# Kernel optimization log

Measured on AMD Instinct MI355X. Metric: run time of the kernel, lower is better.

The kernel has to match this reference:

```python
import jax, jax.numpy as jnp
import numpy as np

B, N, NSAMPLE = 8, 2048, 32
D = 64          # input feature channels
C1, C2 = 64, 128  # MLP channels (channels list after +3 on input: 67 -> 64 -> 128)
RADIUS = 0.15
EPS = 1e-5


def setup_inputs() -> dict:
    key = jax.random.key(0)
    ks = jax.random.split(key, 4)
    position = jax.random.uniform(ks[0], (B, N, 3), dtype=jnp.float32)
    feature = jax.random.normal(ks[1], (B, N, D), dtype=jnp.float32)
    W1 = jax.random.normal(ks[2], (D + 3, C1), dtype=jnp.float32) * 0.05
    gamma1 = jnp.ones((C1,), jnp.float32)
    beta1 = jnp.zeros((C1,), jnp.float32)
    W2 = jax.random.normal(ks[3], (C1, C2), dtype=jnp.float32) * 0.05
    gamma2 = jnp.ones((C2,), jnp.float32)
    beta2 = jnp.zeros((C2,), jnp.float32)
    return {"position": position, "feature": feature,
            "W1": W1, "gamma1": gamma1, "beta1": beta1,
            "W2": W2, "gamma2": gamma2, "beta2": beta2}


def _ball_query(xyz, radius, nsample):
    # squared pairwise distances [B, N, N]
    sq = (jnp.sum(xyz ** 2, -1)[:, :, None]
          + jnp.sum(xyz ** 2, -1)[:, None, :]
          - 2.0 * jnp.einsum('bnc,bmc->bnm', xyz, xyz))
    n = xyz.shape[1]
    idx = jnp.where(sq > radius ** 2, n, jnp.arange(n, dtype=jnp.int32)[None, None, :])
    idx = jnp.sort(idx, axis=-1)[:, :, :nsample]            # [B, N, nsample]
    first = idx[:, :, :1]
    return jnp.where(idx == n, first, idx)                  # pad misses with first neighbor


def _gather(points, idx):
    # points [B, N, C], idx [B, S, K] -> [B, S, K, C]
    b, s, k = idx.shape
    flat = jnp.take_along_axis(points, idx.reshape(b, s * k, 1), axis=1)
    return flat.reshape(b, s, k, points.shape[-1])


def _bn_relu(x, gamma, beta, relu=True):
    # BatchNorm1d over channel dim (train-mode stats across B*N*S), per linearblock
    mean = jnp.mean(x, axis=(0, 1, 2), keepdims=True)
    var = jnp.var(x, axis=(0, 1, 2), keepdims=True)
    y = (x - mean) * jax.lax.rsqrt(var + EPS) * gamma + beta
    return jax.nn.relu(y) if relu else y


def reference(position, feature, W1, gamma1, beta1, W2, gamma2, beta2):
    b, n, _ = position.shape
    idx = _ball_query(position, RADIUS, NSAMPLE)            # [B, N, nsample]
    grouped_xyz = _gather(position, idx) - position[:, :, None, :]  # [B,N,ns,3]
    grouped_feat = _gather(feature, idx)                    # [B, N, ns, D]
    h = jnp.concatenate([grouped_xyz, grouped_feat], axis=-1)  # [B, N, ns, 3+D]
    h = _bn_relu(h @ W1, gamma1, beta1)                     # [B, N, ns, C1]
    h = _bn_relu(h @ W2, gamma2, beta2)                     # [B, N, ns, C2]
    new_feature = jnp.max(h, axis=2)                        # [B, N, C2]
    return position, new_feature
```

## Files before the change

### kernel.cpp

```cpp
#include <hip/hip_runtime.h>
#include <hip/hip_bf16.h>


#define BB 8
#define NN 2048
#define KK 32
#define DD 64
#define CC1 64
#define CC2 128
#define TOTROWS (BB*NN*KK)
#define SITES (BB*NN)
#define PSLICES 256
#define DBLOCKS 4096

typedef __bf16 bf16x8 __attribute__((ext_vector_type(8)));
typedef float  f32x4  __attribute__((ext_vector_type(4)));

__device__ __forceinline__ void lds_add(float* p, float v) {
  __hip_atomic_fetch_add(p, v, __ATOMIC_RELAXED, __HIP_MEMORY_SCOPE_WORKGROUP);
}

__global__ __launch_bounds__(256) void k1_ball(const float* __restrict__ pos,
                                               int* __restrict__ idx)
{
  __shared__ float4 P[NN];
  const int b = blockIdx.x >> 6;
  const int qbase = (blockIdx.x & 63) * 32;
  for (int i = threadIdx.x; i < NN; i += 256) {
    const float* p = pos + ((size_t)b*NN + i)*3;
    float x = p[0], y = p[1], z = p[2];
    float s = __fadd_rn(__fadd_rn(__fmul_rn(x,x), __fmul_rn(y,y)), __fmul_rn(z,z));
    P[i] = make_float4(x, y, z, s);
  }
  __syncthreads();
  const int wave = threadIdx.x >> 6, lane = threadIdx.x & 63;
  const float R2 = (float)(0.15 * 0.15);
  const unsigned long long lt = (lane == 63) ? 0x7fffffffffffffffull
                                             : ((1ull << lane) - 1ull);
  for (int qi = wave; qi < 32; qi += 4) {
    const int q = qbase + qi;
    const float4 Q = P[q];
    int* ip = idx + ((size_t)b*NN + q)*KK;
    int cnt = 0, first = -1;
    for (int step = 0; step < 32; ++step) {
      float4 p = P[step*64 + lane];
      float d = __fmul_rn(Q.x, p.x);
      d = fmaf(Q.y, p.y, d);
      d = fmaf(Q.z, p.z, d);
      float sq = __fsub_rn(__fadd_rn(Q.w, p.w), __fmul_rn(2.0f, d));
      bool in = !(sq > R2);
      unsigned long long mask = __ballot(in);
      if (first < 0 && mask) first = step*64 + (int)__builtin_ctzll(mask);
      int dst = cnt + (int)__popcll(mask & lt);
      if (in && dst < KK) ip[dst] = step*64 + lane;
      cnt += (int)__popcll(mask);
      if (cnt >= KK) break;
    }
    if (lane >= cnt && lane < KK) ip[lane] = first;
  }
}

__global__ __launch_bounds__(1024, 1) void kP_scatter(
    const float* __restrict__ pos, const int* __restrict__ idx,
    float* __restrict__ Pc, float* __restrict__ Px,
    float* __restrict__ Py, float* __restrict__ Pz,
    float* __restrict__ momP)
{
  __shared__ unsigned int Sc[NN], Sx[NN], Sy[NN], Sz[NN];
  __shared__ float mred[16*9];
  const int b = blockIdx.x >> 5;
  const int slice = blockIdx.x & 31;
  for (int i = threadIdx.x; i < NN; i += 1024) {
    Sc[i] = 0u; Sx[i] = 0u; Sy[i] = 0u; Sz[i] = 0u;
  }
  __syncthreads();
  const float* pb = pos + (size_t)b*NN*3;
  const int sl = threadIdx.x >> 4;
  const int kg = threadIdx.x & 15;
  const int site = slice*64 + sl;
  const int* ip = idx + ((size_t)(b*NN + site))*KK;
  const int ip0 = ip[0];
  const float cx = pb[site*3], cy = pb[site*3+1], cz = pb[site*3+2];
  const float FS = 4194304.0f;
  float m1x=0.f,m1y=0.f,m1z=0.f,mxx=0.f,myy=0.f,mzz=0.f,mxy=0.f,mxz=0.f,myz=0.f;
  int wt = 0;
  #pragma unroll
  for (int j = 0; j < 2; ++j) {
    const int k = kg*2 + j;
    const int m = ip[k];
    float dx = pb[m*3  ] - cx;
    float dy = pb[m*3+1] - cy;
    float dz = pb[m*3+2] - cz;
    if (k > 0 && m == ip0) {
      ++wt;
    } else {
      atomicAdd(&Sc[m], 1u);
      atomicAdd(&Sx[m], (unsigned int)__float2int_rn(dx*FS));
      atomicAdd(&Sy[m], (unsigned int)__float2int_rn(dy*FS));
      atomicAdd(&Sz[m], (unsigned int)__float2int_rn(dz*FS));
    }
    m1x += dx; m1y += dy; m1z += dz;
    mxx = fmaf(dx,dx,mxx); myy = fmaf(dy,dy,myy); mzz = fmaf(dz,dz,mzz);
    mxy = fmaf(dx,dy,mxy); mxz = fmaf(dx,dz,mxz); myz = fmaf(dy,dz,myz);
  }
  if (wt > 0) {
    float dx0 = pb[ip0*3  ] - cx;
    float dy0 = pb[ip0*3+1] - cy;
    float dz0 = pb[ip0*3+2] - cz;
    atomicAdd(&Sc[ip0], (unsigned int)wt);
    atomicAdd(&Sx[ip0], (unsigned int)(wt*__float2int_rn(dx0*FS)));
    atomicAdd(&Sy[ip0], (unsigned int)(wt*__float2int_rn(dy0*FS)));
    atomicAdd(&Sz[ip0], (unsigned int)(wt*__float2int_rn(dz0*FS)));
  }
  const int lane = threadIdx.x & 63;
  const int wv = threadIdx.x >> 6;
  float vals[9] = {m1x,m1y,m1z,mxx,myy,mzz,mxy,mxz,myz};
  #pragma unroll
  for (int i = 0; i < 9; ++i) {
    float v = vals[i];
    #pragma unroll
    for (int s = 1; s < 64; s <<= 1) v += __shfl_xor(v, s, 64);
    if (lane == 0) mred[wv*9 + i] = v;
  }
  __syncthreads();
  const float IS = 2.38418579101562500e-7f;
  float* pc = Pc + (size_t)blockIdx.x*NN;
  float* px = Px + (size_t)blockIdx.x*NN;
  float* py = Py + (size_t)blockIdx.x*NN;
  float* pz = Pz + (size_t)blockIdx.x*NN;
  for (int i = threadIdx.x; i < NN; i += 1024) {
    pc[i] = (float)Sc[i];
    px[i] = (float)(int)Sx[i] * IS;
    py[i] = (float)(int)Sy[i] * IS;
    pz[i] = (float)(int)Sz[i] * IS;
  }
  if (threadIdx.x < 9) {
    float s = 0.f;
    #pragma unroll
    for (int w2 = 0; w2 < 16; ++w2) s += mred[w2*9 + threadIdx.x];
    momP[(size_t)blockIdx.x*16 + threadIdx.x] = s;
  }
}

__global__ __launch_bounds__(256) void kR_reduce(
    const float* __restrict__ Pc, const float* __restrict__ Px,
    const float* __restrict__ Py, const float* __restrict__ Pz,
    const float* __restrict__ momP,
    float* __restrict__ cnt, float* __restrict__ DXa,
    float* __restrict__ DYa, float* __restrict__ DZa,
    float* __restrict__ mom)
{
  __shared__ float mr[256];
  if (blockIdx.x == 256) {
    const int t = threadIdx.x;
    const int i = t & 15, j = t >> 4;
    float s = 0.f;
    #pragma unroll
    for (int q = 0; q < 16; ++q) s += momP[(size_t)(j*16 + q)*16 + i];
    mr[t] = s;
    __syncthreads();
    if (t < 16) {
      float tot = 0.f;
      #pragma unroll
      for (int q = 0; q < 16; ++q) tot += mr[q*16 + t];
      if (t < 9) mom[t] = tot;
    }
    return;
  }
  int i = blockIdx.x*256 + threadIdx.x;
  int a = i >> 14;
  int j = i & 16383;
  int b = j >> 11, m = j & (NN-1);
  const float* P = (a == 0) ? Pc : (a == 1) ? Px : (a == 2) ? Py : Pz;
  float s = 0.f;
  #pragma unroll
  for (int sl = 0; sl < 32; ++sl) s += P[(size_t)(b*32 + sl)*NN + m];
  float* O = (a == 0) ? cnt : (a == 1) ? DXa : (a == 2) ? DYa : DZa;
  O[j] = s;
}

__global__ __launch_bounds__(256) void kB_g(const float* __restrict__ feat,
                                            const float* __restrict__ W1,
                                            const float* __restrict__ cnt,
                                            const float* __restrict__ DXa,
                                            const float* __restrict__ DYa,
                                            const float* __restrict__ DZa,
                                            float* __restrict__ g,
                                            float* __restrict__ A_p)
{
  __shared__ float red[320];
  for (int i = threadIdx.x; i < 320; i += 256) red[i] = 0.f;
  __syncthreads();
  const int lane = threadIdx.x & 63;
  const int quad = lane >> 4;
  const int col  = lane & 15;
  const int gw = (blockIdx.x*256 + threadIdx.x) >> 6;

  bf16x8 Bf[2][4];
  #pragma unroll
  for (int kt = 0; kt < 2; ++kt)
    #pragma unroll
    for (int nt = 0; nt < 4; ++nt) {
      bf16x8 v;
      #pragma unroll
      for (int j = 0; j < 8; ++j)
        v[j] = (__bf16)W1[(3 + kt*32 + quad*8 + j)*CC1 + nt*16 + col];
      Bf[kt][nt] = v;
    }
  float a1[4], a2[4], a3[4], a4[4], a5[4];
  #pragma unroll
  for (int nt = 0; nt < 4; ++nt) { a1[nt]=0.f; a2[nt]=0.f; a3[nt]=0.f; a4[nt]=0.f; a5[nt]=0.f; }

  for (int t = 0; t < 2; ++t) {
    const int row0 = (gw*2 + t) * 16;
    bf16x8 Af[2];
    #pragma unroll
    for (int kt = 0; kt < 2; ++kt) {
      const float4* fp =
        (const float4*)(feat + (size_t)(row0 + col)*DD + kt*32 + quad*8);
      float4 f0 = fp[0], f1 = fp[1];
      float fv[8] = {f0.x,f0.y,f0.z,f0.w,f1.x,f1.y,f1.z,f1.w};
      bf16x8 v;
      #pragma unroll
      for (int j = 0; j < 8; ++j) v[j] = (__bf16)fv[j];
      Af[kt] = v;
    }
    float cw[4], dxw[4], dyw[4], dzw[4];
    #pragma unroll
    for (int r = 0; r < 4; ++r) {
      int row = row0 + quad*4 + r;
      cw[r] = cnt[row]; dxw[r] = DXa[row]; dyw[r] = DYa[row]; dzw[r] = DZa[row];
    }
    #pragma unroll
    for (int nt = 0; nt < 4; ++nt) {
      f32x4 a = {0.f, 0.f, 0.f, 0.f};
      a = __builtin_amdgcn_mfma_f32_16x16x32_bf16(Af[0], Bf[0][nt], a, 0, 0, 0);
      a = __builtin_amdgcn_mfma_f32_16x16x32_bf16(Af[1], Bf[1][nt], a, 0, 0, 0);
      #pragma unroll
      for (int r = 0; r < 4; ++r) {
        float v = a[r];
        g[(size_t)(row0 + quad*4 + r)*CC1 + nt*16 + col] = v;
        float cv = cw[r]*v;
        a1[nt] += cv; a2[nt] = fmaf(cv, v, a2[nt]);
        a3[nt] = fmaf(dxw[r], v, a3[nt]);
        a4[nt] = fmaf(dyw[r], v, a4[nt]);
        a5[nt] = fmaf(dzw[r], v, a5[nt]);
      }
    }
  }
  #pragma unroll
  for (int nt = 0; nt < 4; ++nt) {
    float v1=a1[nt], v2=a2[nt], v3=a3[nt], v4=a4[nt], v5=a5[nt];
    v1 += __shfl_xor(v1,16,64); v1 += __shfl_xor(v1,32,64);
    v2 += __shfl_xor(v2,16,64); v2 += __shfl_xor(v2,32,64);
    v3 += __shfl_xor(v3,16,64); v3 += __shfl_xor(v3,32,64);
    v4 += __shfl_xor(v4,16,64); v4 += __shfl_xor(v4,32,64);
    v5 += __shfl_xor(v5,16,64); v5 += __shfl_xor(v5,32,64);
    if (quad == 0) {
      int ch = nt*16 + col;
      lds_add(&red[ch], v1);
      lds_add(&red[64+ch], v2);
      lds_add(&red[128+ch], v3);
      lds_add(&red[192+ch], v4);
      lds_add(&red[256+ch], v5);
    }
  }
  __syncthreads();
  for (int i = threadIdx.x; i < 320; i += 256)
    A_p[(size_t)blockIdx.x*320 + i] = red[i];
}

__global__ __launch_bounds__(256) void kS_fold(
    const float* __restrict__ W1, const float* __restrict__ gamma1,
    const float* __restrict__ beta1, const float* __restrict__ A_p,
    const float* __restrict__ mom, float* __restrict__ A,
    float* __restrict__ sc1, float* __restrict__ sh1, float* __restrict__ W1s)
{
  for (int c = threadIdx.x; c < 320; c += 256) {
    float s = 0.f;
    for (int blk = 0; blk < 128; ++blk) s += A_p[(size_t)blk*320 + c];
    A[c] = s;
  }
  __syncthreads();
  int c = threadIdx.x;
  if (c >= CC1) return;
  float wx = W1[c], wy = W1[CC1+c], wz = W1[2*CC1+c];
  float A1 = A[c], A2 = A[64+c], A3x = A[128+c], A3y = A[192+c], A3z = A[256+c];
  float sum1 = A1 + wx*mom[0] + wy*mom[1] + wz*mom[2];
  float ss = A2 + 2.f*(wx*A3x + wy*A3y + wz*A3z)
           + wx*wx*mom[3] + wy*wy*mom[4] + wz*wz*mom[5]
           + 2.f*(wx*wy*mom[6] + wx*wz*mom[7] + wy*wz*mom[8]);
  const float invN = 1.0f / (float)TOTROWS;
  float mean = sum1 * invN;
  float var  = ss * invN - mean*mean;
  float sc = rsqrtf(var + 1e-5f) * gamma1[c];
  float sh = beta1[c] - mean * sc;
  sc1[c] = sc; sh1[c] = sh;
  W1s[c] = wx*sc; W1s[64+c] = wy*sc; W1s[128+c] = wz*sc;
}

__global__ __launch_bounds__(256, 2) void kD_mfma(
    const float* __restrict__ pos, const int* __restrict__ idx,
    const float* __restrict__ g, const float* __restrict__ sc1,
    const float* __restrict__ sh1, const float* __restrict__ W1s,
    const float* __restrict__ W2,
    float* __restrict__ stats2P, float* __restrict__ out_nf)
{
  __shared__ __bf16 W2T[CC2*72];
  __shared__ float red2[256];
  red2[threadIdx.x] = 0.f;
  {
    const int n  = threadIdx.x & 127;
    const int k0 = (threadIdx.x >> 7) << 5;
    #pragma unroll
    for (int jj = 0; jj < 4; ++jj) {
      unsigned int pk[4];
      #pragma unroll
      for (int q2 = 0; q2 < 4; ++q2) {
        const int k = k0 + jj*8 + q2*2;
        __bf16 lo = (__bf16)W2[(size_t)k*CC2 + n];
        __bf16 hi = (__bf16)W2[(size_t)(k+1)*CC2 + n];
        unsigned short ulo, uhi;
        __builtin_memcpy(&ulo, &lo, 2);
        __builtin_memcpy(&uhi, &hi, 2);
        pk[q2] = ((unsigned int)uhi << 16) | (unsigned int)ulo;
      }
      __builtin_memcpy(&W2T[n*72 + k0 + jj*8], pk, 16);
    }
  }
  __syncthreads();

  const int lane = threadIdx.x & 63;
  const int quad = lane >> 4;
  const int col  = lane & 15;
  const int site = (blockIdx.x*256 + threadIdx.x) >> 6;
  const int b  = site >> 11;
  const int ls = site & (NN-1);
  const float* pb = pos + (size_t)b*NN*3;
  const int* ip = idx + (size_t)site*KK;

  const int ma = ip[col], mb = ip[16 + col];
  const float ccx = pb[ls*3], ccy = pb[ls*3+1], ccz = pb[ls*3+2];
  const float dxa = pb[ma*3]-ccx, dya = pb[ma*3+1]-ccy, dza = pb[ma*3+2]-ccz;
  const float dxb = pb[mb*3]-ccx, dyb = pb[mb*3+1]-ccy, dzb = pb[mb*3+2]-ccz;

  const float* gbase = g + (size_t)b*NN*CC1;
  const float* ra = gbase + (size_t)ma*CC1 + quad*8;
  const float* rb = gbase + (size_t)mb*CC1 + quad*8;
  f32x4 gA0 = *(const f32x4*)ra,      gA1 = *(const f32x4*)(ra+4);
  f32x4 gA2 = *(const f32x4*)(ra+32), gA3 = *(const f32x4*)(ra+36);
  f32x4 gB0 = *(const f32x4*)rb,      gB1 = *(const f32x4*)(rb+4);
  f32x4 gB2 = *(const f32x4*)(rb+32), gB3 = *(const f32x4*)(rb+36);

  bf16x8 A00, A01, A10, A11;
  {
    const int c0 = quad*8;
    f32x4 x0 = *(const f32x4*)&W1s[c0],     x1 = *(const f32x4*)&W1s[c0+4];
    f32x4 y0 = *(const f32x4*)&W1s[64+c0],  y1 = *(const f32x4*)&W1s[64+c0+4];
    f32x4 z0 = *(const f32x4*)&W1s[128+c0], z1 = *(const f32x4*)&W1s[128+c0+4];
    f32x4 s0 = *(const f32x4*)&sc1[c0],     s1 = *(const f32x4*)&sc1[c0+4];
    f32x4 h0 = *(const f32x4*)&sh1[c0],     h1 = *(const f32x4*)&sh1[c0+4];
    #pragma unroll
    for (int j = 0; j < 8; ++j) {
      float wx = (j<4)?x0[j]:x1[j-4], wy = (j<4)?y0[j]:y1[j-4];
      float wz = (j<4)?z0[j]:z1[j-4], sc = (j<4)?s0[j]:s1[j-4];
      float sh = (j<4)?h0[j]:h1[j-4];
      float ga = (j<4)?gA0[j]:gA1[j-4], gb = (j<4)?gB0[j]:gB1[j-4];
      float ta = fmaf(dza, wz, fmaf(dya, wy, fmaf(dxa, wx, sh)));
      A00[j] = (__bf16)fmaxf(fmaf(ga, sc, ta), 0.f);
      float tb = fmaf(dzb, wz, fmaf(dyb, wy, fmaf(dxb, wx, sh)));
      A10[j] = (__bf16)fmaxf(fmaf(gb, sc, tb), 0.f);
    }
  }
  {
    const int c0 = 32 + quad*8;
    f32x4 x0 = *(const f32x4*)&W1s[c0],     x1 = *(const f32x4*)&W1s[c0+4];
    f32x4 y0 = *(const f32x4*)&W1s[64+c0],  y1 = *(const f32x4*)&W1s[64+c0+4];
    f32x4 z0 = *(const f32x4*)&W1s[128+c0], z1 = *(const f32x4*)&W1s[128+c0+4];
    f32x4 s0 = *(const f32x4*)&sc1[c0],     s1 = *(const f32x4*)&sc1[c0+4];
    f32x4 h0 = *(const f32x4*)&sh1[c0],     h1 = *(const f32x4*)&sh1[c0+4];
    #pragma unroll
    for (int j = 0; j < 8; ++j) {
      float wx = (j<4)?x0[j]:x1[j-4], wy = (j<4)?y0[j]:y1[j-4];
      float wz = (j<4)?z0[j]:z1[j-4], sc = (j<4)?s0[j]:s1[j-4];
      float sh = (j<4)?h0[j]:h1[j-4];
      float ga = (j<4)?gA2[j]:gA3[j-4], gb = (j<4)?gB2[j]:gB3[j-4];
      float ta = fmaf(dza, wz, fmaf(dya, wy, fmaf(dxa, wx, sh)));
      A01[j] = (__bf16)fmaxf(fmaf(ga, sc, ta), 0.f);
      float tb = fmaf(dzb, wz, fmaf(dyb, wy, fmaf(dxb, wx, sh)));
      A11[j] = (__bf16)fmaxf(fmaf(gb, sc, tb), 0.f);
    }
  }

  float ssum[8], ssq[8];
  #pragma unroll
  for (int nt = 0; nt < 8; ++nt) { ssum[nt] = 0.f; ssq[nt] = 0.f; }

  float* outp = out_nf + (size_t)site*CC2;
  #pragma unroll
  for (int nt = 0; nt < 8; ++nt) {
    const bf16x8 B0 = *(const bf16x8*)&W2T[(nt*16 + col)*72 + quad*8];
    const bf16x8 B1 = *(const bf16x8*)&W2T[(nt*16 + col)*72 + 32 + quad*8];
    float mxv = -3.0e38f;
    f32x4 a = {0.f, 0.f, 0.f, 0.f};
    a = __builtin_amdgcn_mfma_f32_16x16x32_bf16(A00, B0, a, 0, 0, 0);
    a = __builtin_amdgcn_mfma_f32_16x16x32_bf16(A01, B1, a, 0, 0, 0);
    #pragma unroll
    for (int r = 0; r < 4; ++r) {
      float v = a[r];
      ssum[nt] += v; ssq[nt] = fmaf(v, v, ssq[nt]); mxv = fmaxf(mxv, v);
    }
    f32x4 a2 = {0.f, 0.f, 0.f, 0.f};
    a2 = __builtin_amdgcn_mfma_f32_16x16x32_bf16(A10, B0, a2, 0, 0, 0);
    a2 = __builtin_amdgcn_mfma_f32_16x16x32_bf16(A11, B1, a2, 0, 0, 0);
    #pragma unroll
    for (int r = 0; r < 4; ++r) {
      float v = a2[r];
      ssum[nt] += v; ssq[nt] = fmaf(v, v, ssq[nt]); mxv = fmaxf(mxv, v);
    }
    mxv = fmaxf(mxv, __shfl_xor(mxv, 16, 64));
    mxv = fmaxf(mxv, __shfl_xor(mxv, 32, 64));
    if ((nt & 3) == quad) outp[nt*16 + col] = mxv;
  }

  #pragma unroll
  for (int nt = 0; nt < 8; ++nt) {
    float s = ssum[nt];
    s += __shfl_xor(s, 16, 64); s += __shfl_xor(s, 32, 64);
    float q = ssq[nt];
    q += __shfl_xor(q, 16, 64); q += __shfl_xor(q, 32, 64);
    if (lane < 16) {
      atomicAdd(&red2[nt*16 + col], s);
      atomicAdd(&red2[128 + nt*16 + col], q);
    }
  }
  __syncthreads();
  stats2P[(size_t)blockIdx.x*256 + threadIdx.x] = red2[threadIdx.x];
}

__global__ __launch_bounds__(256) void kR2_stats(
    const float* __restrict__ stats2P, float* __restrict__ stats2)
{
  __shared__ float r[256];
  const int c = blockIdx.x;
  float s = 0.f;
  for (int i = threadIdx.x; i < DBLOCKS; i += 256)
    s += stats2P[(size_t)i*256 + c];
  r[threadIdx.x] = s;
  __syncthreads();
  for (int off = 128; off > 0; off >>= 1) {
    if (threadIdx.x < off) r[threadIdx.x] += r[threadIdx.x + off];
    __syncthreads();
  }
  if (threadIdx.x == 0) stats2[c] = r[0];
}

__global__ __launch_bounds__(256) void k45_epi(const float* __restrict__ pos,
                                               const float* __restrict__ g2,
                                               const float* __restrict__ be2,
                                               const float* __restrict__ stats2,
                                               float* __restrict__ out)
{
  int i = blockIdx.x*256 + threadIdx.x;
  if (blockIdx.x < 192) { out[i] = pos[i]; return; }
  int j = i - 192*256;
  int c = j & (CC2-1);
  const float invc = 1.0f / (float)TOTROWS;
  float mean = stats2[c] * invc;
  float var  = stats2[128 + c] * invc - mean*mean;
  float sc = rsqrtf(var + 1e-5f) * g2[c];
  float sh = be2[c] - mean * sc;
  float* out_nf = out + (size_t)BB*NN*3;
  float x = out_nf[j];
  out_nf[j] = fmaxf(fmaf(x, sc, sh), 0.f);
}

extern "C" void kernel_launch(void* const* d_in, const int* in_sizes, int n_in,
                              void* d_out, int out_size, void* d_ws, size_t ws_size,
                              hipStream_t stream) {
  const float* pos  = (const float*)d_in[0];
  const float* feat = (const float*)d_in[1];
  const float* W1   = (const float*)d_in[2];
  const float* g1   = (const float*)d_in[3];
  const float* be1  = (const float*)d_in[4];
  const float* W2   = (const float*)d_in[5];
  const float* g2   = (const float*)d_in[6];
  const float* be2  = (const float*)d_in[7];
  float* out = (float*)d_out;
  float* out_nf = out + (size_t)BB*NN*3;

  char* w = (char*)d_ws;
  int*   idx    = (int*)w;
  float* A      = (float*)(w + 0x200000);
  float* mom    = A + 320;
  float* stats2 = mom + 16;
  float* sc1    = stats2 + 256;
  float* sh1    = sc1 + 64;
  float* W1s    = sh1 + 64;
  float* cnt    = (float*)(w + 0x210000);
  float* DXa    = cnt + SITES;
  float* DYa    = DXa + SITES;
  float* DZa    = DYa + SITES;
  float* momP   = (float*)(w + 0x250000);
  float* Pc     = (float*)(w + 0x260000);
  float* Px     = Pc + (size_t)PSLICES*NN;
  float* Py     = Px + (size_t)PSLICES*NN;
  float* Pz     = Py + (size_t)PSLICES*NN;
  float* g      = (float*)(w + 0x260000);
  float* A_p    = (float*)(w + 0x660000);
  float* stats2P= (float*)(w + 0x660000);

  k1_ball   <<<512, 256, 0, stream>>>(pos, idx);
  kP_scatter<<<256, 1024, 0, stream>>>(pos, idx, Pc, Px, Py, Pz, momP);
  kR_reduce <<<257, 256, 0, stream>>>(Pc, Px, Py, Pz, momP,
                                      cnt, DXa, DYa, DZa, mom);
  kB_g      <<<128, 256, 0, stream>>>(feat, W1, cnt, DXa, DYa, DZa, g, A_p);
  kS_fold   <<<1, 256, 0, stream>>>(W1, g1, be1, A_p, mom, A, sc1, sh1, W1s);
  kD_mfma   <<<DBLOCKS, 256, 0, stream>>>(pos, idx, g, sc1, sh1, W1s, W2,
                                          stats2P, out_nf);
  kR2_stats <<<256, 256, 0, stream>>>(stats2P, stats2);
  k45_epi   <<<192 + (SITES*CC2)/256, 256, 0, stream>>>(pos, g2, be2, stats2, out);
}
```

Measured before the change: 199.1 us.

## Fold reduction kernels into producers via last-block atomics; process four sites per wave

```diff
diff --git a/kernel.cpp b/kernel.cpp
--- a/kernel.cpp
+++ b/kernel.cpp
@@ -11,7 +11,7 @@
 #define TOTROWS (BB*NN*KK)
 #define SITES (BB*NN)
 #define PSLICES 256
-#define DBLOCKS 4096
+#define DBLOCKS 1024
 
 typedef __bf16 bf16x8 __attribute__((ext_vector_type(8)));
 typedef float  f32x4  __attribute__((ext_vector_type(4)));
@@ -64,10 +64,13 @@
     const float* __restrict__ pos, const int* __restrict__ idx,
     float* __restrict__ Pc, float* __restrict__ Px,
     float* __restrict__ Py, float* __restrict__ Pz,
-    float* __restrict__ momP)
+    float* __restrict__ momP, int* __restrict__ doneP,
+    float* __restrict__ cnt, float* __restrict__ DXa,
+    float* __restrict__ DYa, float* __restrict__ DZa)
 {
   __shared__ unsigned int Sc[NN], Sx[NN], Sy[NN], Sz[NN];
   __shared__ float mred[16*9];
+  __shared__ int lastB;
   const int b = blockIdx.x >> 5;
   const int slice = blockIdx.x & 31;
   for (int i = threadIdx.x; i < NN; i += 1024) {
@@ -140,55 +143,47 @@
     for (int w2 = 0; w2 < 16; ++w2) s += mred[w2*9 + threadIdx.x];
     momP[(size_t)blockIdx.x*16 + threadIdx.x] = s;
   }
-}
-
-__global__ __launch_bounds__(256) void kR_reduce(
-    const float* __restrict__ Pc, const float* __restrict__ Px,
-    const float* __restrict__ Py, const float* __restrict__ Pz,
-    const float* __restrict__ momP,
-    float* __restrict__ cnt, float* __restrict__ DXa,
-    float* __restrict__ DYa, float* __restrict__ DZa,
-    float* __restrict__ mom)
-{
-  __shared__ float mr[256];
-  if (blockIdx.x == 256) {
-    const int t = threadIdx.x;
-    const int i = t & 15, j = t >> 4;
-    float s = 0.f;
-    #pragma unroll
-    for (int q = 0; q < 16; ++q) s += momP[(size_t)(j*16 + q)*16 + i];
-    mr[t] = s;
-    __syncthreads();
-    if (t < 16) {
-      float tot = 0.f;
-      #pragma unroll
-      for (int q = 0; q < 16; ++q) tot += mr[q*16 + t];
-      if (t < 9) mom[t] = tot;
-    }
-    return;
-  }
-  int i = blockIdx.x*256 + threadIdx.x;
-  int a = i >> 14;
-  int j = i & 16383;
-  int b = j >> 11, m = j & (NN-1);
-  const float* P = (a == 0) ? Pc : (a == 1) ? Px : (a == 2) ? Py : Pz;
-  float s = 0.f;
-  #pragma unroll
-  for (int sl = 0; sl < 32; ++sl) s += P[(size_t)(b*32 + sl)*NN + m];
-  float* O = (a == 0) ? cnt : (a == 1) ? DXa : (a == 2) ? DYa : DZa;
-  O[j] = s;
+  __threadfence();
+  if (threadIdx.x == 0) {
+    int old = __hip_atomic_fetch_add(&doneP[b], 1,
+                                     __ATOMIC_ACQ_REL, __HIP_MEMORY_SCOPE_AGENT);
+    lastB = (old == 31);
+  }
+  __syncthreads();
+  if (lastB) {
+    for (int j = threadIdx.x; j < 4*NN; j += 1024) {
+      const int a = j >> 11, m = j & (NN-1);
+      const float* P = (a == 0) ? Pc : (a == 1) ? Px : (a == 2) ? Py : Pz;
+      float s = 0.f;
+      #pragma unroll
+      for (int q = 0; q < 32; ++q) s += P[(size_t)(b*32 + q)*NN + m];
+      float* O = (a == 0) ? cnt : (a == 1) ? DXa : (a == 2) ? DYa : DZa;
+      O[b*NN + m] = s;
+    }
+  }
 }
 
 __global__ __launch_bounds__(256) void kB_g(const float* __restrict__ feat,
                                             const float* __restrict__ W1,
+                                            const float* __restrict__ gamma1,
+                                            const float* __restrict__ beta1,
                                             const float* __restrict__ cnt,
                                             const float* __restrict__ DXa,
                                             const float* __restrict__ DYa,
                                             const float* __restrict__ DZa,
+                                            const float* __restrict__ momP,
                                             float* __restrict__ g,
-                                            float* __restrict__ A_p)
+                                            float* __restrict__ A_p,
+                                            int* __restrict__ doneB,
+                                            float* __restrict__ sc1,
+                                            float* __restrict__ sh1,
+                                            float* __restrict__ W1s)
 {
   __shared__ float red[320];
+  __shared__ float mr[256];
+  __shared__ float momL[16];
+  __shared__ float AL[320];
+  __shared__ int lastF;
   for (int i = threadIdx.x; i < 320; i += 256) red[i] = 0.f;
   __syncthreads();
   const int lane = threadIdx.x & 63;
@@ -268,35 +263,53 @@
   __syncthreads();
   for (int i = threadIdx.x; i < 320; i += 256)
     A_p[(size_t)blockIdx.x*320 + i] = red[i];
-}
-
-__global__ __launch_bounds__(256) void kS_fold(
-    const float* __restrict__ W1, const float* __restrict__ gamma1,
-    const float* __restrict__ beta1, const float* __restrict__ A_p,
-    const float* __restrict__ mom, float* __restrict__ A,
-    float* __restrict__ sc1, float* __restrict__ sh1, float* __restrict__ W1s)
-{
-  for (int c = threadIdx.x; c < 320; c += 256) {
-    float s = 0.f;
-    for (int blk = 0; blk < 128; ++blk) s += A_p[(size_t)blk*320 + c];
-    A[c] = s;
-  }
-  __syncthreads();
-  int c = threadIdx.x;
-  if (c >= CC1) return;
-  float wx = W1[c], wy = W1[CC1+c], wz = W1[2*CC1+c];
-  float A1 = A[c], A2 = A[64+c], A3x = A[128+c], A3y = A[192+c], A3z = A[256+c];
-  float sum1 = A1 + wx*mom[0] + wy*mom[1] + wz*mom[2];
-  float ss = A2 + 2.f*(wx*A3x + wy*A3y + wz*A3z)
-           + wx*wx*mom[3] + wy*wy*mom[4] + wz*wz*mom[5]
-           + 2.f*(wx*wy*mom[6] + wx*wz*mom[7] + wy*wz*mom[8]);
-  const float invN = 1.0f / (float)TOTROWS;
-  float mean = sum1 * invN;
-  float var  = ss * invN - mean*mean;
-  float sc = rsqrtf(var + 1e-5f) * gamma1[c];
-  float sh = beta1[c] - mean * sc;
-  sc1[c] = sc; sh1[c] = sh;
-  W1s[c] = wx*sc; W1s[64+c] = wy*sc; W1s[128+c] = wz*sc;
+  __threadfence();
+  if (threadIdx.x == 0) {
+    int old = __hip_atomic_fetch_add(doneB, 1,
+                                     __ATOMIC_ACQ_REL, __HIP_MEMORY_SCOPE_AGENT);
+    lastF = (old == 127);
+  }
+  __syncthreads();
+  if (lastF) {
+    {
+      const int t = threadIdx.x;
+      const int i = t & 15, jq = t >> 4;
+      float s = 0.f;
+      #pragma unroll
+      for (int q = 0; q < 16; ++q) s += momP[(size_t)(jq*16 + q)*16 + i];
+      mr[t] = s;
+    }
+    __syncthreads();
+    if (threadIdx.x < 16) {
+      float tot = 0.f;
+      #pragma unroll
+      for (int q = 0; q < 16; ++q) tot += mr[q*16 + threadIdx.x];
+      momL[threadIdx.x] = tot;
+    }
+    for (int c = threadIdx.x; c < 320; c += 256) {
+      float s = 0.f;
+      for (int blk = 0; blk < 128; ++blk) s += A_p[(size_t)blk*320 + c];
+      AL[c] = s;
+    }
+    __syncthreads();
+    const int c = threadIdx.x;
+    if (c < CC1) {
+      float wx = W1[c], wy = W1[CC1+c], wz = W1[2*CC1+c];
+      float A1 = AL[c], A2 = AL[64+c];
+      float A3x = AL[128+c], A3y = AL[192+c], A3z = AL[256+c];
+      float sum1 = A1 + wx*momL[0] + wy*momL[1] + wz*momL[2];
+      float ss = A2 + 2.f*(wx*A3x + wy*A3y + wz*A3z)
+               + wx*wx*momL[3] + wy*wy*momL[4] + wz*wz*momL[5]
+               + 2.f*(wx*wy*momL[6] + wx*wz*momL[7] + wy*wz*momL[8]);
+      const float invN = 1.0f / (float)TOTROWS;
+      float mean = sum1 * invN;
+      float var  = ss * invN - mean*mean;
+      float sc = rsqrtf(var + 1e-5f) * gamma1[c];
+      float sh = beta1[c] - mean * sc;
+      sc1[c] = sc; sh1[c] = sh;
+      W1s[c] = wx*sc; W1s[64+c] = wy*sc; W1s[128+c] = wz*sc;
+    }
+  }
 }
 
 __global__ __launch_bounds__(256, 2) void kD_mfma(
@@ -333,94 +346,99 @@
   const int lane = threadIdx.x & 63;
   const int quad = lane >> 4;
   const int col  = lane & 15;
-  const int site = (blockIdx.x*256 + threadIdx.x) >> 6;
-  const int b  = site >> 11;
-  const int ls = site & (NN-1);
-  const float* pb = pos + (size_t)b*NN*3;
-  const int* ip = idx + (size_t)site*KK;
-
-  const int ma = ip[col], mb = ip[16 + col];
-  const float ccx = pb[ls*3], ccy = pb[ls*3+1], ccz = pb[ls*3+2];
-  const float dxa = pb[ma*3]-ccx, dya = pb[ma*3+1]-ccy, dza = pb[ma*3+2]-ccz;
-  const float dxb = pb[mb*3]-ccx, dyb = pb[mb*3+1]-ccy, dzb = pb[mb*3+2]-ccz;
-
-  const float* gbase = g + (size_t)b*NN*CC1;
-  const float* ra = gbase + (size_t)ma*CC1 + quad*8;
-  const float* rb = gbase + (size_t)mb*CC1 + quad*8;
-  f32x4 gA0 = *(const f32x4*)ra,      gA1 = *(const f32x4*)(ra+4);
-  f32x4 gA2 = *(const f32x4*)(ra+32), gA3 = *(const f32x4*)(ra+36);
-  f32x4 gB0 = *(const f32x4*)rb,      gB1 = *(const f32x4*)(rb+4);
-  f32x4 gB2 = *(const f32x4*)(rb+32), gB3 = *(const f32x4*)(rb+36);
-
-  bf16x8 A00, A01, A10, A11;
-  {
-    const int c0 = quad*8;
-    f32x4 x0 = *(const f32x4*)&W1s[c0],     x1 = *(const f32x4*)&W1s[c0+4];
-    f32x4 y0 = *(const f32x4*)&W1s[64+c0],  y1 = *(const f32x4*)&W1s[64+c0+4];
-    f32x4 z0 = *(const f32x4*)&W1s[128+c0], z1 = *(const f32x4*)&W1s[128+c0+4];
-    f32x4 s0 = *(const f32x4*)&sc1[c0],     s1 = *(const f32x4*)&sc1[c0+4];
-    f32x4 h0 = *(const f32x4*)&sh1[c0],     h1 = *(const f32x4*)&sh1[c0+4];
-    #pragma unroll
-    for (int j = 0; j < 8; ++j) {
-      float wx = (j<4)?x0[j]:x1[j-4], wy = (j<4)?y0[j]:y1[j-4];
-      float wz = (j<4)?z0[j]:z1[j-4], sc = (j<4)?s0[j]:s1[j-4];
-      float sh = (j<4)?h0[j]:h1[j-4];
-      float ga = (j<4)?gA0[j]:gA1[j-4], gb = (j<4)?gB0[j]:gB1[j-4];
-      float ta = fmaf(dza, wz, fmaf(dya, wy, fmaf(dxa, wx, sh)));
-      A00[j] = (__bf16)fmaxf(fmaf(ga, sc, ta), 0.f);
-      float tb = fmaf(dzb, wz, fmaf(dyb, wy, fmaf(dxb, wx, sh)));
-      A10[j] = (__bf16)fmaxf(fmaf(gb, sc, tb), 0.f);
-    }
-  }
-  {
-    const int c0 = 32 + quad*8;
-    f32x4 x0 = *(const f32x4*)&W1s[c0],     x1 = *(const f32x4*)&W1s[c0+4];
-    f32x4 y0 = *(const f32x4*)&W1s[64+c0],  y1 = *(const f32x4*)&W1s[64+c0+4];
-    f32x4 z0 = *(const f32x4*)&W1s[128+c0], z1 = *(const f32x4*)&W1s[128+c0+4];
-    f32x4 s0 = *(const f32x4*)&sc1[c0],     s1 = *(const f32x4*)&sc1[c0+4];
-    f32x4 h0 = *(const f32x4*)&sh1[c0],     h1 = *(const f32x4*)&sh1[c0+4];
-    #pragma unroll
-    for (int j = 0; j < 8; ++j) {
-      float wx = (j<4)?x0[j]:x1[j-4], wy = (j<4)?y0[j]:y1[j-4];
-      float wz = (j<4)?z0[j]:z1[j-4], sc = (j<4)?s0[j]:s1[j-4];
-      float sh = (j<4)?h0[j]:h1[j-4];
-      float ga = (j<4)?gA2[j]:gA3[j-4], gb = (j<4)?gB2[j]:gB3[j-4];
-      float ta = fmaf(dza, wz, fmaf(dya, wy, fmaf(dxa, wx, sh)));
-      A01[j] = (__bf16)fmaxf(fmaf(ga, sc, ta), 0.f);
-      float tb = fmaf(dzb, wz, fmaf(dyb, wy, fmaf(dxb, wx, sh)));
-      A11[j] = (__bf16)fmaxf(fmaf(gb, sc, tb), 0.f);
-    }
-  }
+  const int wv = (blockIdx.x*256 + threadIdx.x) >> 6;
 
   float ssum[8], ssq[8];
   #pragma unroll
   for (int nt = 0; nt < 8; ++nt) { ssum[nt] = 0.f; ssq[nt] = 0.f; }
 
-  float* outp = out_nf + (size_t)site*CC2;
-  #pragma unroll
-  for (int nt = 0; nt < 8; ++nt) {
-    const bf16x8 B0 = *(const bf16x8*)&W2T[(nt*16 + col)*72 + quad*8];
-    const bf16x8 B1 = *(const bf16x8*)&W2T[(nt*16 + col)*72 + 32 + quad*8];
-    float mxv = -3.0e38f;
-    f32x4 a = {0.f, 0.f, 0.f, 0.f};
-    a = __builtin_amdgcn_mfma_f32_16x16x32_bf16(A00, B0, a, 0, 0, 0);
-    a = __builtin_amdgcn_mfma_f32_16x16x32_bf16(A01, B1, a, 0, 0, 0);
-    #pragma unroll
-    for (int r = 0; r < 4; ++r) {
-      float v = a[r];
-      ssum[nt] += v; ssq[nt] = fmaf(v, v, ssq[nt]); mxv = fmaxf(mxv, v);
-    }
-    f32x4 a2 = {0.f, 0.f, 0.f, 0.f};
-    a2 = __builtin_amdgcn_mfma_f32_16x16x32_bf16(A10, B0, a2, 0, 0, 0);
-    a2 = __builtin_amdgcn_mfma_f32_16x16x32_bf16(A11, B1, a2, 0, 0, 0);
-    #pragma unroll
-    for (int r = 0; r < 4; ++r) {
-      float v = a2[r];
-      ssum[nt] += v; ssq[nt] = fmaf(v, v, ssq[nt]); mxv = fmaxf(mxv, v);
-    }
-    mxv = fmaxf(mxv, __shfl_xor(mxv, 16, 64));
-    mxv = fmaxf(mxv, __shfl_xor(mxv, 32, 64));
-    if ((nt & 3) == quad) outp[nt*16 + col] = mxv;
+  #pragma clang loop unroll(disable)
+  for (int si = 0; si < 4; ++si) {
+    const int site = wv*4 + si;
+    const int b  = site >> 11;
+    const int ls = site & (NN-1);
+    const float* pb = pos + (size_t)b*NN*3;
+    const int* ip = idx + (size_t)site*KK;
+
+    const int ma = ip[col], mb = ip[16 + col];
+    const float ccx = pb[ls*3], ccy = pb[ls*3+1], ccz = pb[ls*3+2];
+    const float dxa = pb[ma*3]-ccx, dya = pb[ma*3+1]-ccy, dza = pb[ma*3+2]-ccz;
+    const float dxb = pb[mb*3]-ccx, dyb = pb[mb*3+1]-ccy, dzb = pb[mb*3+2]-ccz;
+
+    const float* gbase = g + (size_t)b*NN*CC1;
+    const float* ra = gbase + (size_t)ma*CC1 + quad*8;
+    const float* rb = gbase + (size_t)mb*CC1 + quad*8;
+    f32x4 gA0 = *(const f32x4*)ra,      gA1 = *(const f32x4*)(ra+4);
+    f32x4 gA2 = *(const f32x4*)(ra+32), gA3 = *(const f32x4*)(ra+36);
+    f32x4 gB0 = *(const f32x4*)rb,      gB1 = *(const f32x4*)(rb+4);
+    f32x4 gB2 = *(const f32x4*)(rb+32), gB3 = *(const f32x4*)(rb+36);
+
+    bf16x8 A00, A01, A10, A11;
+    {
+      const int c0 = quad*8;
+      f32x4 x0 = *(const f32x4*)&W1s[c0],     x1 = *(const f32x4*)&W1s[c0+4];
+      f32x4 y0 = *(const f32x4*)&W1s[64+c0],  y1 = *(const f32x4*)&W1s[64+c0+4];
+      f32x4 z0 = *(const f32x4*)&W1s[128+c0], z1 = *(const f32x4*)&W1s[128+c0+4];
+      f32x4 s0 = *(const f32x4*)&sc1[c0],     s1 = *(const f32x4*)&sc1[c0+4];
+      f32x4 h0 = *(const f32x4*)&sh1[c0],     h1 = *(const f32x4*)&sh1[c0+4];
+      #pragma unroll
+      for (int j = 0; j < 8; ++j) {
+        float wx = (j<4)?x0[j]:x1[j-4], wy = (j<4)?y0[j]:y1[j-4];
+        float wz = (j<4)?z0[j]:z1[j-4], sc = (j<4)?s0[j]:s1[j-4];
+        float sh = (j<4)?h0[j]:h1[j-4];
+        float ga = (j<4)?gA0[j]:gA1[j-4], gb = (j<4)?gB0[j]:gB1[j-4];
+        float ta = fmaf(dza, wz, fmaf(dya, wy, fmaf(dxa, wx, sh)));
+        A00[j] = (__bf16)fmaxf(fmaf(ga, sc, ta), 0.f);
+        float tb = fmaf(dzb, wz, fmaf(dyb, wy, fmaf(dxb, wx, sh)));
+        A10[j] = (__bf16)fmaxf(fmaf(gb, sc, tb), 0.f);
+      }
+    }
+    {
+      const int c0 = 32 + quad*8;
+      f32x4 x0 = *(const f32x4*)&W1s[c0],     x1 = *(const f32x4*)&W1s[c0+4];
+      f32x4 y0 = *(const f32x4*)&W1s[64+c0],  y1 = *(const f32x4*)&W1s[64+c0+4];
+      f32x4 z0 = *(const f32x4*)&W1s[128+c0], z1 = *(const f32x4*)&W1s[128+c0+4];
+      f32x4 s0 = *(const f32x4*)&sc1[c0],     s1 = *(const f32x4*)&sc1[c0+4];
+      f32x4 h0 = *(const f32x4*)&sh1[c0],     h1 = *(const f32x4*)&sh1[c0+4];
+      #pragma unroll
+      for (int j = 0; j < 8; ++j) {
+        float wx = (j<4)?x0[j]:x1[j-4], wy = (j<4)?y0[j]:y1[j-4];
+        float wz = (j<4)?z0[j]:z1[j-4], sc = (j<4)?s0[j]:s1[j-4];
+        float sh = (j<4)?h0[j]:h1[j-4];
+        float ga = (j<4)?gA2[j]:gA3[j-4], gb = (j<4)?gB2[j]:gB3[j-4];
+        float ta = fmaf(dza, wz, fmaf(dya, wy, fmaf(dxa, wx, sh)));
+        A01[j] = (__bf16)fmaxf(fmaf(ga, sc, ta), 0.f);
+        float tb = fmaf(dzb, wz, fmaf(dyb, wy, fmaf(dxb, wx, sh)));
+        A11[j] = (__bf16)fmaxf(fmaf(gb, sc, tb), 0.f);
+      }
+    }
+
+    float* outp = out_nf + (size_t)site*CC2;
+    #pragma unroll
+    for (int nt = 0; nt < 8; ++nt) {
+      const bf16x8 B0 = *(const bf16x8*)&W2T[(nt*16 + col)*72 + quad*8];
+      const bf16x8 B1 = *(const bf16x8*)&W2T[(nt*16 + col)*72 + 32 + quad*8];
+      float mxv = -3.0e38f;
+      f32x4 a = {0.f, 0.f, 0.f, 0.f};
+      a = __builtin_amdgcn_mfma_f32_16x16x32_bf16(A00, B0, a, 0, 0, 0);
+      a = __builtin_amdgcn_mfma_f32_16x16x32_bf16(A01, B1, a, 0, 0, 0);
+      #pragma unroll
+      for (int r = 0; r < 4; ++r) {
+        float v = a[r];
+        ssum[nt] += v; ssq[nt] = fmaf(v, v, ssq[nt]); mxv = fmaxf(mxv, v);
+      }
+      f32x4 a2 = {0.f, 0.f, 0.f, 0.f};
+      a2 = __builtin_amdgcn_mfma_f32_16x16x32_bf16(A10, B0, a2, 0, 0, 0);
+      a2 = __builtin_amdgcn_mfma_f32_16x16x32_bf16(A11, B1, a2, 0, 0, 0);
+      #pragma unroll
+      for (int r = 0; r < 4; ++r) {
+        float v = a2[r];
+        ssum[nt] += v; ssq[nt] = fmaf(v, v, ssq[nt]); mxv = fmaxf(mxv, v);
+      }
+      mxv = fmaxf(mxv, __shfl_xor(mxv, 16, 64));
+      mxv = fmaxf(mxv, __shfl_xor(mxv, 32, 64));
+      if ((nt & 3) == quad) outp[nt*16 + col] = mxv;
+    }
   }
 
   #pragma unroll
@@ -491,12 +509,12 @@
 
   char* w = (char*)d_ws;
   int*   idx    = (int*)w;
-  float* A      = (float*)(w + 0x200000);
-  float* mom    = A + 320;
-  float* stats2 = mom + 16;
+  float* stats2 = (float*)(w + 0x200000);
   float* sc1    = stats2 + 256;
   float* sh1    = sc1 + 64;
   float* W1s    = sh1 + 64;
+  int*   doneP  = (int*)(w + 0x208000);
+  int*   doneB  = doneP + 8;
   float* cnt    = (float*)(w + 0x210000);
   float* DXa    = cnt + SITES;
   float* DYa    = DXa + SITES;
@@ -508,14 +526,14 @@
   float* Pz     = Py + (size_t)PSLICES*NN;
   float* g      = (float*)(w + 0x260000);
   float* A_p    = (float*)(w + 0x660000);
-  float* stats2P= (float*)(w + 0x660000);
-
+  float* stats2P= (float*)(w + 0x6A0000);
+
+  hipMemsetAsync(doneP, 0, 16*sizeof(int), stream);
   k1_ball   <<<512, 256, 0, stream>>>(pos, idx);
-  kP_scatter<<<256, 1024, 0, stream>>>(pos, idx, Pc, Px, Py, Pz, momP);
-  kR_reduce <<<257, 256, 0, stream>>>(Pc, Px, Py, Pz, momP,
-                                      cnt, DXa, DYa, DZa, mom);
-  kB_g      <<<128, 256, 0, stream>>>(feat, W1, cnt, DXa, DYa, DZa, g, A_p);
-  kS_fold   <<<1, 256, 0, stream>>>(W1, g1, be1, A_p, mom, A, sc1, sh1, W1s);
+  kP_scatter<<<256, 1024, 0, stream>>>(pos, idx, Pc, Px, Py, Pz, momP, doneP,
+                                       cnt, DXa, DYa, DZa);
+  kB_g      <<<128, 256, 0, stream>>>(feat, W1, g1, be1, cnt, DXa, DYa, DZa,
+                                      momP, g, A_p, doneB, sc1, sh1, W1s);
   kD_mfma   <<<DBLOCKS, 256, 0, stream>>>(pos, idx, g, sc1, sh1, W1s, W2,
                                           stats2P, out_nf);
   kR2_stats <<<256, 256, 0, stream>>>(stats2P, stats2);
```

Measured after the change: 299.7 us. 50.6% more time.

## Fuse ball query with scatter and fold partial reductions into consumers

Applied to the files above, without the earlier changes.

```diff
diff --git a/kernel.cpp b/kernel.cpp
--- a/kernel.cpp
+++ b/kernel.cpp
@@ -20,27 +20,35 @@
   __hip_atomic_fetch_add(p, v, __ATOMIC_RELAXED, __HIP_MEMORY_SCOPE_WORKGROUP);
 }
 
-__global__ __launch_bounds__(256) void k1_ball(const float* __restrict__ pos,
-                                               int* __restrict__ idx)
+__global__ __launch_bounds__(1024, 1) void kQ_ball_scatter(
+    const float* __restrict__ pos, int* __restrict__ idx,
+    float* __restrict__ Pc, float* __restrict__ Px,
+    float* __restrict__ Py, float* __restrict__ Pz,
+    float* __restrict__ momP)
 {
   __shared__ float4 P[NN];
-  const int b = blockIdx.x >> 6;
-  const int qbase = (blockIdx.x & 63) * 32;
-  for (int i = threadIdx.x; i < NN; i += 256) {
+  __shared__ unsigned int Sc[NN], Sx[NN], Sy[NN], Sz[NN];
+  __shared__ int idxL[64*KK];
+  __shared__ float mred[16*9];
+  const int b = blockIdx.x >> 5;
+  const int slice = blockIdx.x & 31;
+  for (int i = threadIdx.x; i < NN; i += 1024) {
     const float* p = pos + ((size_t)b*NN + i)*3;
     float x = p[0], y = p[1], z = p[2];
     float s = __fadd_rn(__fadd_rn(__fmul_rn(x,x), __fmul_rn(y,y)), __fmul_rn(z,z));
     P[i] = make_float4(x, y, z, s);
+    Sc[i] = 0u; Sx[i] = 0u; Sy[i] = 0u; Sz[i] = 0u;
   }
   __syncthreads();
   const int wave = threadIdx.x >> 6, lane = threadIdx.x & 63;
   const float R2 = (float)(0.15 * 0.15);
   const unsigned long long lt = (lane == 63) ? 0x7fffffffffffffffull
                                              : ((1ull << lane) - 1ull);
-  for (int qi = wave; qi < 32; qi += 4) {
-    const int q = qbase + qi;
+  for (int qi = wave; qi < 64; qi += 16) {
+    const int q = slice*64 + qi;
     const float4 Q = P[q];
     int* ip = idx + ((size_t)b*NN + q)*KK;
+    int* il = idxL + qi*KK;
     int cnt = 0, first = -1;
     for (int step = 0; step < 32; ++step) {
       float4 p = P[step*64 + lane];
@@ -52,45 +60,28 @@
       unsigned long long mask = __ballot(in);
       if (first < 0 && mask) first = step*64 + (int)__builtin_ctzll(mask);
       int dst = cnt + (int)__popcll(mask & lt);
-      if (in && dst < KK) ip[dst] = step*64 + lane;
+      if (in && dst < KK) { ip[dst] = step*64 + lane; il[dst] = step*64 + lane; }
       cnt += (int)__popcll(mask);
       if (cnt >= KK) break;
     }
-    if (lane >= cnt && lane < KK) ip[lane] = first;
-  }
-}
-
-__global__ __launch_bounds__(1024, 1) void kP_scatter(
-    const float* __restrict__ pos, const int* __restrict__ idx,
-    float* __restrict__ Pc, float* __restrict__ Px,
-    float* __restrict__ Py, float* __restrict__ Pz,
-    float* __restrict__ momP)
-{
-  __shared__ unsigned int Sc[NN], Sx[NN], Sy[NN], Sz[NN];
-  __shared__ float mred[16*9];
-  const int b = blockIdx.x >> 5;
-  const int slice = blockIdx.x & 31;
-  for (int i = threadIdx.x; i < NN; i += 1024) {
-    Sc[i] = 0u; Sx[i] = 0u; Sy[i] = 0u; Sz[i] = 0u;
-  }
-  __syncthreads();
-  const float* pb = pos + (size_t)b*NN*3;
+    if (lane >= cnt && lane < KK) { ip[lane] = first; il[lane] = first; }
+  }
+  __syncthreads();
   const int sl = threadIdx.x >> 4;
   const int kg = threadIdx.x & 15;
-  const int site = slice*64 + sl;
-  const int* ip = idx + ((size_t)(b*NN + site))*KK;
-  const int ip0 = ip[0];
-  const float cx = pb[site*3], cy = pb[site*3+1], cz = pb[site*3+2];
+  const int ip0 = idxL[sl*KK];
+  const float4 C = P[slice*64 + sl];
   const float FS = 4194304.0f;
   float m1x=0.f,m1y=0.f,m1z=0.f,mxx=0.f,myy=0.f,mzz=0.f,mxy=0.f,mxz=0.f,myz=0.f;
   int wt = 0;
   #pragma unroll
   for (int j = 0; j < 2; ++j) {
     const int k = kg*2 + j;
-    const int m = ip[k];
-    float dx = pb[m*3  ] - cx;
-    float dy = pb[m*3+1] - cy;
-    float dz = pb[m*3+2] - cz;
+    const int m = idxL[sl*KK + k];
+    const float4 Pm = P[m];
+    float dx = Pm.x - C.x;
+    float dy = Pm.y - C.y;
+    float dz = Pm.z - C.z;
     if (k > 0 && m == ip0) {
       ++wt;
     } else {
@@ -104,15 +95,15 @@
     mxy = fmaf(dx,dy,mxy); mxz = fmaf(dx,dz,mxz); myz = fmaf(dy,dz,myz);
   }
   if (wt > 0) {
-    float dx0 = pb[ip0*3  ] - cx;
-    float dy0 = pb[ip0*3+1] - cy;
-    float dz0 = pb[ip0*3+2] - cz;
+    const float4 P0 = P[ip0];
+    float dx0 = P0.x - C.x;
+    float dy0 = P0.y - C.y;
+    float dz0 = P0.z - C.z;
     atomicAdd(&Sc[ip0], (unsigned int)wt);
     atomicAdd(&Sx[ip0], (unsigned int)(wt*__float2int_rn(dx0*FS)));
     atomicAdd(&Sy[ip0], (unsigned int)(wt*__float2int_rn(dy0*FS)));
     atomicAdd(&Sz[ip0], (unsigned int)(wt*__float2int_rn(dz0*FS)));
   }
-  const int lane = threadIdx.x & 63;
   const int wv = threadIdx.x >> 6;
   float vals[9] = {m1x,m1y,m1z,mxx,myy,mzz,mxy,mxz,myz};
   #pragma unroll
@@ -142,54 +133,30 @@
   }
 }
 
-__global__ __launch_bounds__(256) void kR_reduce(
-    const float* __restrict__ Pc, const float* __restrict__ Px,
-    const float* __restrict__ Py, const float* __restrict__ Pz,
-    const float* __restrict__ momP,
-    float* __restrict__ cnt, float* __restrict__ DXa,
-    float* __restrict__ DYa, float* __restrict__ DZa,
-    float* __restrict__ mom)
-{
-  __shared__ float mr[256];
-  if (blockIdx.x == 256) {
-    const int t = threadIdx.x;
-    const int i = t & 15, j = t >> 4;
-    float s = 0.f;
-    #pragma unroll
-    for (int q = 0; q < 16; ++q) s += momP[(size_t)(j*16 + q)*16 + i];
-    mr[t] = s;
-    __syncthreads();
-    if (t < 16) {
-      float tot = 0.f;
-      #pragma unroll
-      for (int q = 0; q < 16; ++q) tot += mr[q*16 + t];
-      if (t < 9) mom[t] = tot;
-    }
-    return;
-  }
-  int i = blockIdx.x*256 + threadIdx.x;
-  int a = i >> 14;
-  int j = i & 16383;
-  int b = j >> 11, m = j & (NN-1);
-  const float* P = (a == 0) ? Pc : (a == 1) ? Px : (a == 2) ? Py : Pz;
-  float s = 0.f;
-  #pragma unroll
-  for (int sl = 0; sl < 32; ++sl) s += P[(size_t)(b*32 + sl)*NN + m];
-  float* O = (a == 0) ? cnt : (a == 1) ? DXa : (a == 2) ? DYa : DZa;
-  O[j] = s;
-}
-
 __global__ __launch_bounds__(256) void kB_g(const float* __restrict__ feat,
                                             const float* __restrict__ W1,
-                                            const float* __restrict__ cnt,
-                                            const float* __restrict__ DXa,
-                                            const float* __restrict__ DYa,
-                                            const float* __restrict__ DZa,
+                                            const float* __restrict__ Pc,
+                                            const float* __restrict__ Px,
+                                            const float* __restrict__ Py,
+                                            const float* __restrict__ Pz,
                                             float* __restrict__ g,
                                             float* __restrict__ A_p)
 {
   __shared__ float red[320];
+  __shared__ float cntL[128], dxL[128], dyL[128], dzL[128];
   for (int i = threadIdx.x; i < 320; i += 256) red[i] = 0.f;
+  const int row0B = blockIdx.x * 128;
+  const int bb = row0B >> 11;
+  for (int r2 = threadIdx.x; r2 < 128; r2 += 256) {
+    const int m = (row0B + r2) & (NN-1);
+    float s0 = 0.f, s1 = 0.f, s2 = 0.f, s3 = 0.f;
+    #pragma unroll 4
+    for (int q = 0; q < 32; ++q) {
+      const size_t base = (size_t)(bb*32 + q)*NN + m;
+      s0 += Pc[base]; s1 += Px[base]; s2 += Py[base]; s3 += Pz[base];
+    }
+    cntL[r2] = s0; dxL[r2] = s1; dyL[r2] = s2; dzL[r2] = s3;
+  }
   __syncthreads();
   const int lane = threadIdx.x & 63;
   const int quad = lane >> 4;
@@ -228,8 +195,8 @@
     float cw[4], dxw[4], dyw[4], dzw[4];
     #pragma unroll
     for (int r = 0; r < 4; ++r) {
-      int row = row0 + quad*4 + r;
-      cw[r] = cnt[row]; dxw[r] = DXa[row]; dyw[r] = DYa[row]; dzw[r] = DZa[row];
+      int rl = row0 - row0B + quad*4 + r;
+      cw[r] = cntL[rl]; dxw[r] = dxL[rl]; dyw[r] = dyL[rl]; dzw[r] = dzL[rl];
     }
     #pragma unroll
     for (int nt = 0; nt < 4; ++nt) {
@@ -273,23 +240,42 @@
 __global__ __launch_bounds__(256) void kS_fold(
     const float* __restrict__ W1, const float* __restrict__ gamma1,
     const float* __restrict__ beta1, const float* __restrict__ A_p,
-    const float* __restrict__ mom, float* __restrict__ A,
+    const float* __restrict__ momP,
     float* __restrict__ sc1, float* __restrict__ sh1, float* __restrict__ W1s)
 {
+  __shared__ float AL[320];
+  __shared__ float mr[256];
+  __shared__ float momL[16];
+  {
+    const int t = threadIdx.x;
+    const int i = t & 15, jq = t >> 4;
+    float s = 0.f;
+    #pragma unroll
+    for (int q = 0; q < 16; ++q) s += momP[(size_t)(jq*16 + q)*16 + i];
+    mr[t] = s;
+  }
   for (int c = threadIdx.x; c < 320; c += 256) {
     float s = 0.f;
     for (int blk = 0; blk < 128; ++blk) s += A_p[(size_t)blk*320 + c];
-    A[c] = s;
-  }
-  __syncthreads();
-  int c = threadIdx.x;
+    AL[c] = s;
+  }
+  __syncthreads();
+  if (threadIdx.x < 16) {
+    float tot = 0.f;
+    #pragma unroll
+    for (int q = 0; q < 16; ++q) tot += mr[q*16 + threadIdx.x];
+    momL[threadIdx.x] = tot;
+  }
+  __syncthreads();
+  const int c = threadIdx.x;
   if (c >= CC1) return;
   float wx = W1[c], wy = W1[CC1+c], wz = W1[2*CC1+c];
-  float A1 = A[c], A2 = A[64+c], A3x = A[128+c], A3y = A[192+c], A3z = A[256+c];
-  float sum1 = A1 + wx*mom[0] + wy*mom[1] + wz*mom[2];
+  float A1 = AL[c], A2 = AL[64+c];
+  float A3x = AL[128+c], A3y = AL[192+c], A3z = AL[256+c];
+  float sum1 = A1 + wx*momL[0] + wy*momL[1] + wz*momL[2];
   float ss = A2 + 2.f*(wx*A3x + wy*A3y + wz*A3z)
-           + wx*wx*mom[3] + wy*wy*mom[4] + wz*wz*mom[5]
-           + 2.f*(wx*wy*mom[6] + wx*wz*mom[7] + wy*wz*mom[8]);
+           + wx*wx*momL[3] + wy*wy*momL[4] + wz*wz*momL[5]
+           + 2.f*(wx*wy*momL[6] + wx*wz*momL[7] + wy*wz*momL[8]);
   const float invN = 1.0f / (float)TOTROWS;
   float mean = sum1 * invN;
   float var  = ss * invN - mean*mean;
@@ -491,31 +477,22 @@
 
   char* w = (char*)d_ws;
   int*   idx    = (int*)w;
-  float* A      = (float*)(w + 0x200000);
-  float* mom    = A + 320;
-  float* stats2 = mom + 16;
+  float* stats2 = (float*)(w + 0x200000);
   float* sc1    = stats2 + 256;
   float* sh1    = sc1 + 64;
   float* W1s    = sh1 + 64;
-  float* cnt    = (float*)(w + 0x210000);
-  float* DXa    = cnt + SITES;
-  float* DYa    = DXa + SITES;
-  float* DZa    = DYa + SITES;
+  float* A_p    = (float*)(w + 0x210000);
   float* momP   = (float*)(w + 0x250000);
   float* Pc     = (float*)(w + 0x260000);
   float* Px     = Pc + (size_t)PSLICES*NN;
   float* Py     = Px + (size_t)PSLICES*NN;
   float* Pz     = Py + (size_t)PSLICES*NN;
-  float* g      = (float*)(w + 0x260000);
-  float* A_p    = (float*)(w + 0x660000);
   float* stats2P= (float*)(w + 0x660000);
-
-  k1_ball   <<<512, 256, 0, stream>>>(pos, idx);
-  kP_scatter<<<256, 1024, 0, stream>>>(pos, idx, Pc, Px, Py, Pz, momP);
-  kR_reduce <<<257, 256, 0, stream>>>(Pc, Px, Py, Pz, momP,
-                                      cnt, DXa, DYa, DZa, mom);
-  kB_g      <<<128, 256, 0, stream>>>(feat, W1, cnt, DXa, DYa, DZa, g, A_p);
-  kS_fold   <<<1, 256, 0, stream>>>(W1, g1, be1, A_p, mom, A, sc1, sh1, W1s);
+  float* g      = (float*)(w + 0xA60000);
+
+  kQ_ball_scatter<<<256, 1024, 0, stream>>>(pos, idx, Pc, Px, Py, Pz, momP);
+  kB_g      <<<128, 256, 0, stream>>>(feat, W1, Pc, Px, Py, Pz, g, A_p);
+  kS_fold   <<<1, 256, 0, stream>>>(W1, g1, be1, A_p, momP, sc1, sh1, W1s);
   kD_mfma   <<<DBLOCKS, 256, 0, stream>>>(pos, idx, g, sc1, sh1, W1s, W2,
                                           stats2P, out_nf);
   kR2_stats <<<256, 256, 0, stream>>>(stats2P, stats2);
```

Result: faster. 187.0 us (-6.1%).
